# Optimization experiments

Measured on AMD Instinct MI355X. Metric: run time of the kernel, lower is better.

Reference implementation:

```python
import jax, jax.numpy as jnp
import numpy as np
from jax.ops import segment_sum

N_NODES = 50000
N_EDGES = 800000
D_IN, D_HID, D_OUT = 128, 128, 64


def setup_inputs() -> dict:
    key = jax.random.key(0)
    ks = jax.random.split(key, 7)
    return {
        "src": jax.random.randint(ks[0], (N_EDGES,), 0, N_NODES, dtype=jnp.int32),
        "dst": jax.random.randint(ks[1], (N_EDGES,), 0, N_NODES, dtype=jnp.int32),
        "x": jax.random.normal(ks[2], (N_NODES, D_IN), dtype=jnp.float32),
        "W1": jax.random.normal(ks[3], (D_IN, D_HID), dtype=jnp.float32) * (1.0 / np.sqrt(D_IN)),
        "b1": jnp.zeros((D_HID,), dtype=jnp.float32),
        "W2": jax.random.normal(ks[4], (D_HID, D_OUT), dtype=jnp.float32) * (1.0 / np.sqrt(D_HID)),
        "b2": jnp.zeros((D_OUT,), dtype=jnp.float32),
    }


def _gcn_layer(src, dst, x, W, b, inv_sqrt_out, inv_sqrt_in):
    # DGL GraphConv, norm='both': h = D_in^{-1/2} A D_out^{-1/2} (x W) + b
    h = (x * inv_sqrt_out[:, None]) @ W          # transform first (in >= out)
    msg = h[src]                                  # gather source messages [E, d]
    agg = segment_sum(msg, dst, num_segments=x.shape[0])
    return agg * inv_sqrt_in[:, None] + b


def reference(src, dst, x, W1, b1, W2, b2):
    n = x.shape[0]
    ones = jnp.ones((src.shape[0],), dtype=x.dtype)
    deg_out = jnp.clip(segment_sum(ones, src, num_segments=n), 1.0)
    deg_in = jnp.clip(segment_sum(ones, dst, num_segments=n), 1.0)
    inv_sqrt_out = jax.lax.rsqrt(deg_out)
    inv_sqrt_in = jax.lax.rsqrt(deg_in)
    h = _gcn_layer(src, dst, x, W1, b1, inv_sqrt_out, inv_sqrt_in)
    h = jax.nn.relu(h)
    h = _gcn_layer(src, dst, h, W2, b2, inv_sqrt_out, inv_sqrt_in)
    return h
```

## Files before the change

kernel.cpp:

```cpp
#include <hip/hip_runtime.h>
#include <hip/hip_fp16.h>

#define D_IN  128
#define D_HID 128
#define D_OUT 64
#define NBMAX 512
#define CHUNK 2048
#define FCACHE 3072

typedef __attribute__((ext_vector_type(8))) short bf16x8;
typedef __attribute__((ext_vector_type(4))) float f32x4;

__device__ __forceinline__ unsigned short f2bf_rne(float f) {
    unsigned int u = __float_as_uint(f);
    return (unsigned short)((u + 0x7FFFu + ((u >> 16) & 1u)) >> 16);
}

__launch_bounds__(256)
__global__ void k_prep(const float* __restrict__ W1, const float* __restrict__ W2,
                       unsigned short* __restrict__ W1h, unsigned short* __restrict__ W1l,
                       unsigned short* __restrict__ W2h, unsigned short* __restrict__ W2l,
                       int* __restrict__ cntD, int* __restrict__ cntS, int NB) {
    const int b = blockIdx.x, t = threadIdx.x;
    if (b < 64) {
        const int i = b * 256 + t;
        const int k = i >> 7, j = i & 127;
        const float v = W1[i];
        const unsigned short hb = f2bf_rne(v);
        const float hf = __uint_as_float((unsigned int)hb << 16);
        W1h[j * 128 + k] = hb;
        W1l[j * 128 + k] = f2bf_rne(v - hf);
    } else if (b < 96) {
        const int i = (b - 64) * 256 + t;
        const int k = i >> 6, j = i & 63;
        const float v = W2[i];
        const unsigned short hb = f2bf_rne(v);
        const float hf = __uint_as_float((unsigned int)hb << 16);
        W2h[j * 128 + k] = hb;
        W2l[j * 128 + k] = f2bf_rne(v - hf);
    } else {
        for (int i = t; i < NB; i += 256) { cntD[i] = 0; cntS[i] = 0; }
    }
}

__launch_bounds__(256)
__global__ void k_bucket(const int* __restrict__ src, const int* __restrict__ dst,
                         int E, int NB, int cap,
                         int* __restrict__ cntD, int* __restrict__ cntS,
                         unsigned int* __restrict__ storeD, unsigned char* __restrict__ storeS) {
    __shared__ int lcD[NBMAX], lcS[NBMAX];
    __shared__ int lbD[NBMAX], lbS[NBMAX];
    const int t = threadIdx.x;
    const int e0 = blockIdx.x * CHUNK;
    const int e1 = min(e0 + CHUNK, E);

    int sv[8], dv[8];
#pragma unroll
    for (int u = 0; u < 8; ++u) {
        const int i = e0 + u * 256 + t;
        if (i < e1) { sv[u] = src[i]; dv[u] = dst[i]; }
        else        { sv[u] = -1;     dv[u] = -1; }
    }

    for (int i = t; i < NB; i += 256) { lcD[i] = 0; lcS[i] = 0; }
    __syncthreads();
#pragma unroll
    for (int u = 0; u < 8; ++u) {
        if (sv[u] >= 0) {
            atomicAdd(&lcD[dv[u] >> 7], 1);
            atomicAdd(&lcS[sv[u] >> 7], 1);
        }
    }
    __syncthreads();
    for (int i = t; i < NB; i += 256) {
        lbD[i] = lcD[i] ? atomicAdd(&cntD[i], lcD[i]) : 0;
        lbS[i] = lcS[i] ? atomicAdd(&cntS[i], lcS[i]) : 0;
        lcD[i] = 0; lcS[i] = 0;
    }
    __syncthreads();
#pragma unroll
    for (int u = 0; u < 8; ++u) {
        if (sv[u] >= 0) {
            const int s = sv[u], d = dv[u];
            const int bd = d >> 7;
            const int pd = lbD[bd] + atomicAdd(&lcD[bd], 1);
            storeD[(long long)bd * cap + pd] = (unsigned int)s | ((unsigned int)(d & 127) << 16);
            const int bs = s >> 7;
            const int ps = lbS[bs] + atomicAdd(&lcS[bs], 1);
            storeS[(long long)bs * cap + ps] = (unsigned char)(s & 127);
        }
    }
}

__launch_bounds__(256)
__global__ void k_fin(const unsigned int* __restrict__ storeD, const unsigned char* __restrict__ storeS,
                      const int* __restrict__ cntD, const int* __restrict__ cntS,
                      int cap, int N, int NB, int E,
                      int* __restrict__ rowptr, float* __restrict__ inv_in,
                      float* __restrict__ inv_out, unsigned short* __restrict__ csr_src) {
    __shared__ int fh[128];
    __shared__ int sc[128];
    __shared__ int cur[128];
    __shared__ int red[256];
    __shared__ unsigned int ecache[FCACHE];
    const int b = blockIdx.x, t = threadIdx.x;
    const long long sb = (long long)b * cap;

    int partial = 0;
    for (int i = t; i < b; i += 256) partial += cntD[i];
    red[t] = partial;
    __syncthreads();
    for (int off = 128; off > 0; off >>= 1) {
        if (t < off) red[t] += red[t + off];
        __syncthreads();
    }
    const int base = red[0];

    const int cnt = cntD[b];
    const bool cached = (cnt <= FCACHE);
    if (cached) {
        for (int i = t; i < cnt; i += 256) ecache[i] = storeD[sb + i];
    }

    if (t < 128) fh[t] = 0;
    __syncthreads();
    for (int i = t; i < cnt; i += 256) {
        const unsigned int e = cached ? ecache[i] : storeD[sb + i];
        atomicAdd(&fh[e >> 16], 1);
    }
    __syncthreads();
    if (t < 128) sc[t] = fh[t];
    __syncthreads();
    int inc = (t < 128) ? sc[t] : 0;
    for (int off = 1; off < 128; off <<= 1) {
        int o = (t >= off && t < 128) ? sc[t - off] : 0;
        __syncthreads();
        if (t < 128) { inc += o; sc[t] = inc; }
        __syncthreads();
    }
    if (t < 128) {
        const int excl = inc - fh[t];
        cur[t] = excl;
        const int node = (b << 7) + t;
        if (node < N) {
            rowptr[node] = base + excl;
            inv_in[node] = rsqrtf((float)max(fh[t], 1));
        }
    }
    if (b == NB - 1 && t == 128) rowptr[N] = E;
    __syncthreads();
    for (int i = t; i < cnt; i += 256) {
        const unsigned int e = cached ? ecache[i] : storeD[sb + i];
        const int pos = atomicAdd(&cur[e >> 16], 1);
        csr_src[base + pos] = (unsigned short)(e & 0xFFFFu);
    }

    __syncthreads();
    if (t < 128) fh[t] = 0;
    __syncthreads();
    const int cnts = cntS[b];
    for (int i = t; i < cnts; i += 256) atomicAdd(&fh[storeS[sb + i]], 1);
    __syncthreads();
    if (t < 128) {
        const int node = (b << 7) + t;
        if (node < N) inv_out[node] = rsqrtf((float)max(fh[t], 1));
    }
}

template<int LDN, typename TA>
__launch_bounds__(256)
__global__ void k_gemm_mfma(const TA* __restrict__ X,
                            const unsigned short* __restrict__ Wth,
                            const unsigned short* __restrict__ Wtl,
                            const float* __restrict__ scale, __half* __restrict__ Y, int N) {
    __shared__ short Ah[32][136], Al[32][136];

    const int t = threadIdx.x;
    const int row0 = blockIdx.x * 32;

    if constexpr (sizeof(TA) == 4) {
#pragma unroll
        for (int p = 0; p < 4; ++p) {
            const int idx = p * 256 + t;
            const int r   = idx >> 5;
            const int c4  = (idx & 31) << 2;
            const int gr  = row0 + r;
            float4 v = make_float4(0.f, 0.f, 0.f, 0.f);
            if (gr < N) {
                v = *(const float4*)((const float*)X + (long long)gr * 128 + c4);
                if (scale) { const float s = scale[gr]; v.x *= s; v.y *= s; v.z *= s; v.w *= s; }
            }
            const float f[4] = {v.x, v.y, v.z, v.w};
            short hh[4], ll[4];
#pragma unroll
            for (int i = 0; i < 4; ++i) {
                const unsigned short hb = f2bf_rne(f[i]);
                const float hf = __uint_as_float(((unsigned int)hb) << 16);
                hh[i] = (short)hb;
                ll[i] = (short)f2bf_rne(f[i] - hf);
            }
            *(short4*)&Ah[r][c4] = make_short4(hh[0], hh[1], hh[2], hh[3]);
            *(short4*)&Al[r][c4] = make_short4(ll[0], ll[1], ll[2], ll[3]);
        }
    } else {
#pragma unroll
        for (int p = 0; p < 2; ++p) {
            const int idx = p * 256 + t;
            const int r   = idx >> 4;
            const int c8  = (idx & 15) << 3;
            const int gr  = row0 + r;
            uint4 raw = make_uint4(0u, 0u, 0u, 0u);
            if (gr < N) raw = *(const uint4*)((const __half*)X + (long long)gr * 128 + c8);
            const __half2* hp = (const __half2*)&raw;
            short hh[8], ll[8];
#pragma unroll
            for (int u = 0; u < 4; ++u) {
                const float2 f2 = __half22float2(hp[u]);
                const float f[2] = {f2.x, f2.y};
#pragma unroll
                for (int q = 0; q < 2; ++q) {
                    const unsigned short hb = f2bf_rne(f[q]);
                    const float hf = __uint_as_float(((unsigned int)hb) << 16);
                    hh[2 * u + q] = (short)hb;
                    ll[2 * u + q] = (short)f2bf_rne(f[q] - hf);
                }
            }
            *(short4*)&Ah[r][c8]     = make_short4(hh[0], hh[1], hh[2], hh[3]);
            *(short4*)&Ah[r][c8 + 4] = make_short4(hh[4], hh[5], hh[6], hh[7]);
            *(short4*)&Al[r][c8]     = make_short4(ll[0], ll[1], ll[2], ll[3]);
            *(short4*)&Al[r][c8 + 4] = make_short4(ll[4], ll[5], ll[6], ll[7]);
        }
    }
    __syncthreads();

    constexpr int NT = LDN / 32;
    const int w    = t >> 6;
    const int lane = t & 63;
    const int rg = w & 1, cg = w >> 1;
    const int lrow = lane & 15;
    const int lk   = (lane >> 4) << 3;
    const int colbase = cg * (16 * NT);

    f32x4 acc[NT];
#pragma unroll
    for (int n = 0; n < NT; ++n) acc[n] = (f32x4){0.f, 0.f, 0.f, 0.f};

#pragma unroll
    for (int ks = 0; ks < 4; ++ks) {
        const int k = ks * 32 + lk;
        const bf16x8 ah = *(const bf16x8*)&Ah[rg * 16 + lrow][k];
        const bf16x8 al = *(const bf16x8*)&Al[rg * 16 + lrow][k];
#pragma unroll
        for (int n = 0; n < NT; ++n) {
            const int col = colbase + n * 16 + lrow;
            const bf16x8 bh = *(const bf16x8*)(Wth + (size_t)col * 128 + k);
            const bf16x8 bl = *(const bf16x8*)(Wtl + (size_t)col * 128 + k);
            acc[n] = __builtin_amdgcn_mfma_f32_16x16x32_bf16(ah, bh, acc[n], 0, 0, 0);
            acc[n] = __builtin_amdgcn_mfma_f32_16x16x32_bf16(ah, bl, acc[n], 0, 0, 0);
            acc[n] = __builtin_amdgcn_mfma_f32_16x16x32_bf16(al, bh, acc[n], 0, 0, 0);
        }
    }

#pragma unroll
    for (int n = 0; n < NT; ++n) {
#pragma unroll
        for (int i = 0; i < 4; ++i) {
            const int r = row0 + rg * 16 + ((lane >> 4) << 2) + i;
            if (r < N)
                Y[(long long)r * LDN + colbase + n * 16 + lrow] = __float2half(acc[n][i]);
        }
    }
}

template<int D, bool RELU, typename TO>
__launch_bounds__(256)
__global__ void k_gather(const int* __restrict__ rowptr, const unsigned short* __restrict__ csr_src,
                         const __half* __restrict__ Y, const float* __restrict__ inv_in,
                         const float* __restrict__ inv_out, const float* __restrict__ b,
                         TO* __restrict__ out, int N) {
    const int wid  = (int)((blockIdx.x * 256u + threadIdx.x) >> 6);
    const int lane = threadIdx.x & 63;
    if (wid >= N) return;

    const int start = rowptr[wid];
    const int end   = rowptr[wid + 1];

    constexpr int LPE = D / 8;
    constexpr int EPW = 64 / LPE;
    const int grp  = lane / LPE;
    const int colh = (lane % LPE) * 8;

    float a[8];
#pragma unroll
    for (int u = 0; u < 8; ++u) a[u] = 0.0f;

    auto accum = [&](uint4 raw) {
        const __half2* h = (const __half2*)&raw;
#pragma unroll
        for (int u = 0; u < 4; ++u) {
            const float2 f = __half22float2(h[u]);
            a[2 * u]     += f.x;
            a[2 * u + 1] += f.y;
        }
    };

    for (int k = start; k < end; k += 64) {
        const int idx = k + lane;
        const int sv  = (idx < end) ? (int)csr_src[idx] : 0;
        const int cnt = min(64, end - k);
        int j = 0;
        for (; j + 4 * EPW <= cnt; j += 4 * EPW) {
            const int s0 = __shfl(sv, j + grp);
            const int s1 = __shfl(sv, j + EPW + grp);
            const int s2 = __shfl(sv, j + 2 * EPW + grp);
            const int s3 = __shfl(sv, j + 3 * EPW + grp);
            const uint4 r0 = *(const uint4*)(Y + (long long)s0 * D + colh);
            const uint4 r1 = *(const uint4*)(Y + (long long)s1 * D + colh);
            const uint4 r2 = *(const uint4*)(Y + (long long)s2 * D + colh);
            const uint4 r3 = *(const uint4*)(Y + (long long)s3 * D + colh);
            accum(r0); accum(r1); accum(r2); accum(r3);
        }
        for (; j < cnt; j += EPW) {
            const int jj = j + grp;
            const int s  = __shfl(sv, jj);
            if (jj < cnt) {
                const uint4 r = *(const uint4*)(Y + (long long)s * D + colh);
                accum(r);
            }
        }
    }

#pragma unroll
    for (int u = 0; u < 8; ++u) a[u] += __shfl_down(a[u], 32);
#pragma unroll
    for (int u = 0; u < 8; ++u) a[u] += __shfl_down(a[u], 16);
    if (EPW == 8) {
#pragma unroll
        for (int u = 0; u < 8; ++u) a[u] += __shfl_down(a[u], 8);
    }

    if (lane < LPE) {
        const float ii = inv_in[wid];
        const float io = RELU ? inv_out[wid] : 0.0f;
        const float4 b0 = *(const float4*)(b + colh);
        const float4 b1 = *(const float4*)(b + colh + 4);
        float r[8];
        r[0] = a[0] * ii + b0.x; r[1] = a[1] * ii + b0.y;
        r[2] = a[2] * ii + b0.z; r[3] = a[3] * ii + b0.w;
        r[4] = a[4] * ii + b1.x; r[5] = a[5] * ii + b1.y;
        r[6] = a[6] * ii + b1.z; r[7] = a[7] * ii + b1.w;
        if (RELU) {
#pragma unroll
            for (int u = 0; u < 8; ++u) r[u] = fmaxf(r[u], 0.0f) * io;
        }
        if constexpr (sizeof(TO) == 2) {
            __half2 h0 = __float22half2_rn(make_float2(r[0], r[1]));
            __half2 h1 = __float22half2_rn(make_float2(r[2], r[3]));
            __half2 h2 = __float22half2_rn(make_float2(r[4], r[5]));
            __half2 h3 = __float22half2_rn(make_float2(r[6], r[7]));
            uint4 pk;
            pk.x = *(unsigned int*)&h0; pk.y = *(unsigned int*)&h1;
            pk.z = *(unsigned int*)&h2; pk.w = *(unsigned int*)&h3;
            *(uint4*)((__half*)out + (long long)wid * D + colh) = pk;
        } else {
            float* o = (float*)out + (long long)wid * D + colh;
            *(float4*)(o)     = make_float4(r[0], r[1], r[2], r[3]);
            *(float4*)(o + 4) = make_float4(r[4], r[5], r[6], r[7]);
        }
    }
}

extern "C" void kernel_launch(void* const* d_in, const int* in_sizes, int n_in,
                              void* d_out, int out_size, void* d_ws, size_t ws_size,
                              hipStream_t stream) {
    const int*   src = (const int*)d_in[0];
    const int*   dst = (const int*)d_in[1];
    const float* x   = (const float*)d_in[2];
    const float* W1  = (const float*)d_in[3];
    const float* b1  = (const float*)d_in[4];
    const float* W2  = (const float*)d_in[5];
    const float* b2  = (const float*)d_in[6];
    float* out = (float*)d_out;

    const int E  = in_sizes[0];
    const int N  = in_sizes[2] / D_IN;
    const int NB = (N + 127) >> 7;
    const int mean = E / NB;
    const int cap  = mean + mean / 4 + 128;

    char* ws = (char*)d_ws;
    size_t off = 0;
    auto alloc = [&](size_t bytes) -> void* {
        void* p = ws + off;
        off += (bytes + 255) & ~(size_t)255;
        return p;
    };
    float*          inv_out = (float*)alloc((size_t)N * 4);
    float*          inv_in  = (float*)alloc((size_t)N * 4);
    int*            rowptr  = (int*)alloc((size_t)(N + 1) * 4);
    int*            cntD    = (int*)alloc((size_t)NB * 4);
    int*            cntS    = (int*)alloc((size_t)NB * 4);
    unsigned int*   storeD  = (unsigned int*)alloc((size_t)NB * cap * 4);
    unsigned char*  storeS  = (unsigned char*)alloc((size_t)NB * cap);
    unsigned short* csr_src = (unsigned short*)alloc((size_t)E * 2);
    unsigned short* W1h     = (unsigned short*)alloc(128 * 128 * 2);
    unsigned short* W1l     = (unsigned short*)alloc(128 * 128 * 2);
    unsigned short* W2h     = (unsigned short*)alloc(64 * 128 * 2);
    unsigned short* W2l     = (unsigned short*)alloc(64 * 128 * 2);
    __half*         Y1      = (__half*)alloc((size_t)N * D_HID * 2);
    __half*         H       = (__half*)alloc((size_t)N * D_HID * 2);
    __half*         Y2      = (__half*)alloc((size_t)N * D_OUT * 2);
    (void)ws_size; (void)n_in; (void)out_size;

    k_prep<<<97, 256, 0, stream>>>(W1, W2, W1h, W1l, W2h, W2l, cntD, cntS, NB);
    k_bucket<<<(E + CHUNK - 1) / CHUNK, 256, 0, stream>>>(src, dst, E, NB, cap, cntD, cntS, storeD, storeS);
    k_fin<<<NB, 256, 0, stream>>>(storeD, storeS, cntD, cntS, cap, N, NB, E,
                                  rowptr, inv_in, inv_out, csr_src);

    k_gemm_mfma<D_HID, float><<<(N + 31) / 32, 256, 0, stream>>>(x, W1h, W1l, inv_out, Y1, N);
    k_gather<D_HID, true, __half><<<(N + 3) / 4, 256, 0, stream>>>(rowptr, csr_src, Y1, inv_in, inv_out, b1, H, N);

    k_gemm_mfma<D_OUT, __half><<<(N + 31) / 32, 256, 0, stream>>>(H, W2h, W2l, nullptr, Y2, N);
    k_gather<D_OUT, false, float><<<(N + 3) / 4, 256, 0, stream>>>(rowptr, csr_src, Y2, inv_in, nullptr, b2, out, N);
}
```

Before: 142.3 us.

## Stage bucketed edges in LDS before scattering, and unroll the gather loop deeper

The bucketing kernel now computes a block-local prefix sum over bucket counts and writes the edge records into shared memory sorted by bucket, together with their global destinations. It then stores them to global memory in a linear loop, so that writes to the same bucket sit close together rather than being scattered per thread. Separately, the aggregation gather loop gains an 8-wide unrolled stage that issues more independent row loads before accumulating, to increase memory-level parallelism. The costs are more shared memory (lower occupancy), extra barriers from the two scans, and higher register pressure in the gather.

```diff
diff --git a/kernel.cpp b/kernel.cpp
--- a/kernel.cpp
+++ b/kernel.cpp
@@ -48,11 +48,19 @@
                          int E, int NB, int cap,
                          int* __restrict__ cntD, int* __restrict__ cntS,
                          unsigned int* __restrict__ storeD, unsigned char* __restrict__ storeS) {
-    __shared__ int lcD[NBMAX], lcS[NBMAX];
-    __shared__ int lbD[NBMAX], lbS[NBMAX];
+    __shared__ int lc[512], ls[512];
+    __shared__ int baD[512], baS[512];
+    __shared__ int gbD[512], gbS[512];
+    __shared__ int ssum[256];
+    __shared__ unsigned int  ldsD[CHUNK];
+    __shared__ int           gposD[CHUNK];
+    __shared__ unsigned char ldsS[CHUNK];
+    __shared__ int           gposS[CHUNK];
+
     const int t = threadIdx.x;
     const int e0 = blockIdx.x * CHUNK;
     const int e1 = min(e0 + CHUNK, E);
+    const int n  = e1 - e0;
 
     int sv[8], dv[8];
 #pragma unroll
@@ -62,33 +70,78 @@
         else        { sv[u] = -1;     dv[u] = -1; }
     }
 
-    for (int i = t; i < NB; i += 256) { lcD[i] = 0; lcS[i] = 0; }
+    lc[t] = 0; lc[t + 256] = 0; ls[t] = 0; ls[t + 256] = 0;
     __syncthreads();
 #pragma unroll
     for (int u = 0; u < 8; ++u) {
         if (sv[u] >= 0) {
-            atomicAdd(&lcD[dv[u] >> 7], 1);
-            atomicAdd(&lcS[sv[u] >> 7], 1);
-        }
-    }
-    __syncthreads();
+            atomicAdd(&lc[dv[u] >> 7], 1);
+            atomicAdd(&ls[sv[u] >> 7], 1);
+        }
+    }
+    __syncthreads();
+
+    const int c0 = lc[2 * t], c1 = lc[2 * t + 1];
+    const int s0 = ls[2 * t], s1 = ls[2 * t + 1];
+    {
+        const int pc = c0 + c1;
+        ssum[t] = pc; __syncthreads();
+        int inc = pc;
+        for (int off = 1; off < 256; off <<= 1) {
+            const int o = (t >= off) ? ssum[t - off] : 0;
+            __syncthreads();
+            inc += o; ssum[t] = inc;
+            __syncthreads();
+        }
+        const int ex = inc - pc;
+        baD[2 * t] = ex; baD[2 * t + 1] = ex + c0;
+    }
+    {
+        const int ps = s0 + s1;
+        ssum[t] = ps; __syncthreads();
+        int inc = ps;
+        for (int off = 1; off < 256; off <<= 1) {
+            const int o = (t >= off) ? ssum[t - off] : 0;
+            __syncthreads();
+            inc += o; ssum[t] = inc;
+            __syncthreads();
+        }
+        const int ex = inc - ps;
+        baS[2 * t] = ex; baS[2 * t + 1] = ex + s0;
+    }
+    __syncthreads();
+
     for (int i = t; i < NB; i += 256) {
-        lbD[i] = lcD[i] ? atomicAdd(&cntD[i], lcD[i]) : 0;
-        lbS[i] = lcS[i] ? atomicAdd(&cntS[i], lcS[i]) : 0;
-        lcD[i] = 0; lcS[i] = 0;
-    }
-    __syncthreads();
+        const int c = lc[i];
+        gbD[i] = i * cap + (c ? atomicAdd(&cntD[i], c) : 0);
+        const int s = ls[i];
+        gbS[i] = i * cap + (s ? atomicAdd(&cntS[i], s) : 0);
+    }
+    __syncthreads();
+    lc[t] = 0; lc[t + 256] = 0; ls[t] = 0; ls[t + 256] = 0;
+    __syncthreads();
+
 #pragma unroll
     for (int u = 0; u < 8; ++u) {
         if (sv[u] >= 0) {
             const int s = sv[u], d = dv[u];
             const int bd = d >> 7;
-            const int pd = lbD[bd] + atomicAdd(&lcD[bd], 1);
-            storeD[(long long)bd * cap + pd] = (unsigned int)s | ((unsigned int)(d & 127) << 16);
+            const int lp = atomicAdd(&lc[bd], 1);
+            const int p  = baD[bd] + lp;
+            ldsD[p]  = (unsigned int)s | ((unsigned int)(d & 127) << 16);
+            gposD[p] = gbD[bd] + lp;
             const int bs = s >> 7;
-            const int ps = lbS[bs] + atomicAdd(&lcS[bs], 1);
-            storeS[(long long)bs * cap + ps] = (unsigned char)(s & 127);
-        }
+            const int lq = atomicAdd(&ls[bs], 1);
+            const int q  = baS[bs] + lq;
+            ldsS[q]  = (unsigned char)(s & 127);
+            gposS[q] = gbS[bs] + lq;
+        }
+    }
+    __syncthreads();
+
+    for (int p = t; p < n; p += 256) {
+        storeD[gposD[p]] = ldsD[p];
+        storeS[gposS[p]] = ldsS[p];
     }
 }
 
@@ -309,16 +362,25 @@
         const int sv  = (idx < end) ? (int)csr_src[idx] : 0;
         const int cnt = min(64, end - k);
         int j = 0;
+        for (; j + 8 * EPW <= cnt; j += 8 * EPW) {
+            int s[8];
+#pragma unroll
+            for (int u = 0; u < 8; ++u) s[u] = __shfl(sv, j + u * EPW + grp);
+            uint4 r[8];
+#pragma unroll
+            for (int u = 0; u < 8; ++u) r[u] = *(const uint4*)(Y + (long long)s[u] * D + colh);
+#pragma unroll
+            for (int u = 0; u < 8; ++u) accum(r[u]);
+        }
         for (; j + 4 * EPW <= cnt; j += 4 * EPW) {
-            const int s0 = __shfl(sv, j + grp);
-            const int s1 = __shfl(sv, j + EPW + grp);
-            const int s2 = __shfl(sv, j + 2 * EPW + grp);
-            const int s3 = __shfl(sv, j + 3 * EPW + grp);
-            const uint4 r0 = *(const uint4*)(Y + (long long)s0 * D + colh);
-            const uint4 r1 = *(const uint4*)(Y + (long long)s1 * D + colh);
-            const uint4 r2 = *(const uint4*)(Y + (long long)s2 * D + colh);
-            const uint4 r3 = *(const uint4*)(Y + (long long)s3 * D + colh);
-            accum(r0); accum(r1); accum(r2); accum(r3);
+            int s[4];
+#pragma unroll
+            for (int u = 0; u < 4; ++u) s[u] = __shfl(sv, j + u * EPW + grp);
+            uint4 r[4];
+#pragma unroll
+            for (int u = 0; u < 4; ++u) r[u] = *(const uint4*)(Y + (long long)s[u] * D + colh);
+#pragma unroll
+            for (int u = 0; u < 4; ++u) accum(r[u]);
         }
         for (; j < cnt; j += EPW) {
             const int jj = j + grp;
```

After: 140.9 us. No clear change (-1.0%).
